# Optimization experiments

Hardware: AMD Instinct MI355X
Metric: run time of the kernel (lower is better)

The kernel has to match this reference:

```python
import jax, jax.numpy as jnp
import numpy as np
import math

B, S, DM, H = 4, 2048, 1024, 16
HD = DM // H

def setup_inputs() -> dict:
    key = jax.random.key(0)
    ks = jax.random.split(key, 12)
    def lin(k, din, dout):
        bound = 1.0 / math.sqrt(din)
        kw, kb = jax.random.split(k)
        W = jax.random.uniform(kw, (din, dout), jnp.float32, -bound, bound)
        b = jax.random.uniform(kb, (dout,), jnp.float32, -bound, bound)
        return W, b
    Wq, bq = lin(ks[0], DM, DM)
    Wk, bk = lin(ks[1], DM, DM)
    Wv, bv = lin(ks[2], DM, DM)
    Wo, bo = lin(ks[3], DM, DM)
    return {
        "Q": jax.random.normal(ks[4], (B, S, DM), jnp.float32),
        "K": jax.random.normal(ks[5], (B, S, DM), jnp.float32),
        "V": jax.random.normal(ks[6], (B, S, DM), jnp.float32),
        "mask": jnp.ones((B, S), jnp.int32),
        "Wq": Wq, "bq": bq, "Wk": Wk, "bk": bk,
        "Wv": Wv, "bv": bv, "Wo": Wo, "bo": bo,
    }

def reference(Q, K, V, mask, Wq, bq, Wk, bk, Wv, bv, Wo, bo):
    N, qlen, dm = Q.shape
    klen = K.shape[1]
    q = (Q @ Wq + bq).reshape(N, qlen, H, HD)
    k = (K @ Wk + bk).reshape(N, klen, H, HD)
    v = (V @ Wv + bv).reshape(N, klen, H, HD)
    # scores: [B, q, H, k]
    dot = jnp.einsum('bqhd,bkhd->bqhk', q, k) / math.sqrt(HD)
    # mask is 2-D (N, klen): broadcast as (N, 1, 1, klen); positions where mask==0 are masked
    m = (mask == 0)[:, None, None, :]
    dot = jnp.where(m, -jnp.inf, dot)
    weights = jax.nn.softmax(dot.astype(jnp.float32), axis=-1).astype(dot.dtype)
    out = jnp.einsum('bqhk,bkhd->bqhd', weights, v).reshape(N, qlen, dm)
    return out @ Wo + bo
```

## Files before the change

kernel.cpp:

```cpp
#include <hip/hip_runtime.h>
#include <math.h>

#define B_  4
#define S_  2048
#define DM_ 1024
#define H_  16
#define HD_ 64

typedef float f32x4 __attribute__((ext_vector_type(4)));
typedef short bf16x8 __attribute__((ext_vector_type(8)));

#define MFMA16(a, b, c) __builtin_amdgcn_mfma_f32_16x16x32_bf16((a), (b), (c), 0, 0, 0)

static __device__ __forceinline__ unsigned short f2bf(float f) {
    union { float f; unsigned int i; } c; c.f = f;
    unsigned int u = c.i;
    return (unsigned short)((u + 0x7fffu + ((u >> 16) & 1u)) >> 16);
}
static __device__ __forceinline__ unsigned int f2u(float f) {
    union { float f; unsigned int u; } c; c.f = f; return c.u;
}
static __device__ __forceinline__ float u2f(unsigned int u) {
    union { unsigned int u; float f; } c; c.u = u; return c.f;
}

static __device__ __forceinline__ void async16(const void* g, void* l) {
    __builtin_amdgcn_global_load_lds(
        (__attribute__((address_space(1))) void*)(void*)g,
        (__attribute__((address_space(3))) void*)l, 16, 0, 0);
}

__global__ __launch_bounds__(256) void cast3_bf16(
    const float* __restrict__ q, const float* __restrict__ k,
    const float* __restrict__ v,
    unsigned short* __restrict__ qo, unsigned short* __restrict__ ko,
    unsigned short* __restrict__ vo) {
    const int z = blockIdx.z;
    const float* in = z == 0 ? q : (z == 1 ? k : v);
    unsigned short* out = z == 0 ? qo : (z == 1 ? ko : vo);
    int idx = (blockIdx.x * 256 + threadIdx.x) * 8;
    float4 a = *(const float4*)(in + idx);
    float4 b = *(const float4*)(in + idx + 4);
    *(ushort4*)(out + idx)     = make_ushort4(f2bf(a.x), f2bf(a.y), f2bf(a.z), f2bf(a.w));
    *(ushort4*)(out + idx + 4) = make_ushort4(f2bf(b.x), f2bf(b.y), f2bf(b.z), f2bf(b.w));
}

__global__ __launch_bounds__(256) void wcast4_t(
    const float* __restrict__ w0, const float* __restrict__ w1,
    const float* __restrict__ w2, const float* __restrict__ w3,
    unsigned short* __restrict__ o0, unsigned short* __restrict__ o1,
    unsigned short* __restrict__ o2, unsigned short* __restrict__ o3) {
    __shared__ float tile[64][65];
    const int z = blockIdx.z;
    const float* W = z == 0 ? w0 : (z == 1 ? w1 : (z == 2 ? w2 : w3));
    unsigned short* Wt = z == 0 ? o0 : (z == 1 ? o1 : (z == 2 ? o2 : o3));
    const int t = threadIdx.x;
    const int k0 = blockIdx.y * 64, n0 = blockIdx.x * 64;
    const int r = t >> 4, c4 = (t & 15) * 4;
    #pragma unroll
    for (int s = 0; s < 4; ++s) {
        float4 f = *(const float4*)(W + (size_t)(k0 + s * 16 + r) * DM_ + n0 + c4);
        tile[s * 16 + r][c4 + 0] = f.x; tile[s * 16 + r][c4 + 1] = f.y;
        tile[s * 16 + r][c4 + 2] = f.z; tile[s * 16 + r][c4 + 3] = f.w;
    }
    __syncthreads();
    #pragma unroll
    for (int s = 0; s < 4; ++s) {
        int n = s * 16 + r;
        ushort4 o = make_ushort4(f2bf(tile[c4 + 0][n]), f2bf(tile[c4 + 1][n]),
                                 f2bf(tile[c4 + 2][n]), f2bf(tile[c4 + 3][n]));
        *(ushort4*)(Wt + (size_t)(n0 + n) * DM_ + k0 + c4) = o;
    }
}

static __device__ __forceinline__ void gemm_body(
    const unsigned short* __restrict__ A,
    const unsigned short* __restrict__ Wt,
    const float* __restrict__ bias,
    void* __restrict__ outp, int mode,
    unsigned short* As, unsigned short* Bs)
{
    const int t = threadIdx.x;
    const int w = t >> 6, l = t & 63;
    const int quad = l >> 4, l16 = l & 15;
    const int wr = w >> 1, wc = w & 1;
    const int m0 = blockIdx.y * 128, n0 = blockIdx.x * 128;

    const int srow = w * 32 + (l >> 2);
    const int scol = (l & 3) * 8;
    const unsigned short* ag = A  + (size_t)(m0 + srow) * DM_ + scol;
    const unsigned short* bg = Wt + (size_t)(n0 + srow) * DM_ + scol;
    unsigned short* al = &As[(w * 32) * 32];
    unsigned short* bl = &Bs[(w * 32) * 32];

    const f32x4 fz = {0.f, 0.f, 0.f, 0.f};
    f32x4 acc[4][4];
    #pragma unroll
    for (int i = 0; i < 4; ++i)
        #pragma unroll
        for (int j = 0; j < 4; ++j) acc[i][j] = fz;

    for (int k0 = 0; k0 < DM_; k0 += 32) {
        __syncthreads();
        async16(ag + k0, al);
        async16(ag + k0 + 16 * DM_, al + 16 * 32);
        async16(bg + k0, bl);
        async16(bg + k0 + 16 * DM_, bl + 16 * 32);
        __syncthreads();
        bf16x8 af[4], bfr[4];
        #pragma unroll
        for (int i = 0; i < 4; ++i)
            af[i] = *(const bf16x8*)&As[(wr * 64 + i * 16 + l16) * 32 + quad * 8];
        #pragma unroll
        for (int j = 0; j < 4; ++j)
            bfr[j] = *(const bf16x8*)&Bs[(wc * 64 + j * 16 + l16) * 32 + quad * 8];
        #pragma unroll
        for (int i = 0; i < 4; ++i)
            #pragma unroll
            for (int j = 0; j < 4; ++j)
                acc[i][j] = MFMA16(af[i], bfr[j], acc[i][j]);
    }

    float bv[4];
    #pragma unroll
    for (int j = 0; j < 4; ++j) bv[j] = bias[n0 + wc * 64 + j * 16 + l16];

    if (mode == 2) {
        float* out = (float*)outp;
        #pragma unroll
        for (int i = 0; i < 4; ++i)
            #pragma unroll
            for (int j = 0; j < 4; ++j) {
                int col = n0 + wc * 64 + j * 16 + l16;
                #pragma unroll
                for (int r = 0; r < 4; ++r) {
                    int row = m0 + wr * 64 + i * 16 + quad * 4 + r;
                    out[(size_t)row * DM_ + col] = acc[i][j][r] + bv[j];
                }
            }
    } else if (mode == 0) {
        unsigned short* out = (unsigned short*)outp;
        #pragma unroll
        for (int i = 0; i < 4; ++i)
            #pragma unroll
            for (int j = 0; j < 4; ++j) {
                int col = n0 + wc * 64 + j * 16 + l16;
                int h = col >> 6, d = col & 63;
                #pragma unroll
                for (int r = 0; r < 4; ++r) {
                    int row = m0 + wr * 64 + i * 16 + quad * 4 + r;
                    int bb = row >> 11, ss = row & (S_ - 1);
                    out[(((size_t)bb * H_ + h) * S_ + ss) * HD_ + d] =
                        f2bf(acc[i][j][r] + bv[j]);
                }
            }
    } else {
        unsigned short* out = (unsigned short*)outp;
        #pragma unroll
        for (int i = 0; i < 4; ++i)
            #pragma unroll
            for (int j = 0; j < 4; ++j) {
                int col = n0 + wc * 64 + j * 16 + l16;
                int h = col >> 6, d = col & 63;
                int row0 = m0 + wr * 64 + i * 16 + quad * 4;
                int bb = row0 >> 11, ss = row0 & (S_ - 1);
                ushort4 o = make_ushort4(f2bf(acc[i][j][0] + bv[j]),
                                         f2bf(acc[i][j][1] + bv[j]),
                                         f2bf(acc[i][j][2] + bv[j]),
                                         f2bf(acc[i][j][3] + bv[j]));
                *(ushort4*)(out + (((size_t)bb * H_ + h) * HD_ + d) * S_ + ss) = o;
            }
    }
}

__global__ __launch_bounds__(256) void gemm_qkv3(
    const unsigned short* __restrict__ Qc, const unsigned short* __restrict__ Kc,
    const unsigned short* __restrict__ Vc,
    const unsigned short* __restrict__ Wqt, const unsigned short* __restrict__ Wkt,
    const unsigned short* __restrict__ Wvt,
    const float* __restrict__ bq, const float* __restrict__ bk,
    const float* __restrict__ bvp,
    unsigned short* __restrict__ qh, unsigned short* __restrict__ kh,
    unsigned short* __restrict__ vth)
{
    __shared__ unsigned short As[128 * 32];
    __shared__ unsigned short Bs[128 * 32];
    const int z = blockIdx.z;
    const unsigned short* A  = z == 0 ? Qc  : (z == 1 ? Kc  : Vc);
    const unsigned short* Wt = z == 0 ? Wqt : (z == 1 ? Wkt : Wvt);
    const float* bias        = z == 0 ? bq  : (z == 1 ? bk  : bvp);
    void* out                = z == 0 ? (void*)qh : (z == 1 ? (void*)kh : (void*)vth);
    gemm_body(A, Wt, bias, out, z == 2 ? 1 : 0, As, Bs);
}

__global__ __launch_bounds__(256) void gemm_omfma(
    const unsigned short* __restrict__ A, const unsigned short* __restrict__ Wt,
    const float* __restrict__ bias, float* __restrict__ out)
{
    __shared__ unsigned short As[128 * 32];
    __shared__ unsigned short Bs[128 * 32];
    gemm_body(A, Wt, bias, out, 2, As, Bs);
}

__global__ __launch_bounds__(256) void attn_mfma(
    const unsigned short* __restrict__ q,
    const unsigned short* __restrict__ k,
    const unsigned short* __restrict__ vt,
    const int* __restrict__ mask,
    unsigned short* __restrict__ out)
{
    __shared__ unsigned short Qs[128 * 64];
    __shared__ unsigned short Ks[64 * 64];
    __shared__ unsigned short Vs[64 * 64];
    __shared__ unsigned short Ps[4][2][16 * 64];
    __shared__ int ms[64];
    const int t = threadIdx.x;
    const int w = t >> 6, l = t & 63;
    const int quad = l >> 4, l16 = l & 15;
    const int b = blockIdx.z, h = blockIdx.y;
    const int q0 = blockIdx.x * 128;
    const size_t hb = ((size_t)b * H_ + h) * S_;
    const float C_ = 0.18033688011112042f;
    const float NINF = -__builtin_inff();

    const unsigned short* qg = q + (hb + q0) * HD_;
    #pragma unroll
    for (int s = 0; s < 4; ++s) {
        int r0 = w * 32 + s * 8;
        int row = r0 + (l >> 3);
        int g = (l & 7) ^ (row & 7);
        async16(qg + (size_t)row * HD_ + g * 8, &Qs[r0 * 64]);
    }
    __syncthreads();
    bf16x8 qf[2][2];
    #pragma unroll
    for (int g = 0; g < 2; ++g)
        #pragma unroll
        for (int c = 0; c < 2; ++c) {
            int row = w * 32 + g * 16 + l16;
            qf[g][c] = *(const bf16x8*)&Qs[row * 64 + (((c * 4 + quad) ^ (row & 7)) * 8)];
        }

    const f32x4 fz = {0.f, 0.f, 0.f, 0.f};
    f32x4 o[2][4];
    float lr[2] = {0.f, 0.f};
    #pragma unroll
    for (int g = 0; g < 2; ++g)
        #pragma unroll
        for (int jv = 0; jv < 4; ++jv) o[g][jv] = fz;

    const unsigned short* kg0 = k + hb * HD_;
    const unsigned short* vg0 = vt + ((size_t)b * H_ + h) * HD_ * S_;

    for (int kt = 0; kt < S_ / 64; ++kt) {
        __syncthreads();
        #pragma unroll
        for (int s = 0; s < 2; ++s) {
            int r0 = w * 16 + s * 8;
            int rr = r0 + (l >> 3);
            int gg = (l & 7) ^ (rr & 7);
            async16(kg0 + (size_t)(kt * 64 + rr) * HD_ + gg * 8, &Ks[r0 * 64]);
            async16(vg0 + (size_t)rr * S_ + kt * 64 + gg * 8, &Vs[r0 * 64]);
        }
        if (t < 64) ms[t] = mask[(size_t)b * S_ + kt * 64 + t];
        __syncthreads();

        float madd[4][4];
        #pragma unroll
        for (int kk = 0; kk < 4; ++kk) {
            int4 mv = *(const int4*)&ms[kk * 16 + quad * 4];
            madd[kk][0] = mv.x ? 0.f : NINF;
            madd[kk][1] = mv.y ? 0.f : NINF;
            madd[kk][2] = mv.z ? 0.f : NINF;
            madd[kk][3] = mv.w ? 0.f : NINF;
        }

        bf16x8 kf[4][2], vfr[4][2];
        #pragma unroll
        for (int kk = 0; kk < 4; ++kk) {
            int row = kk * 16 + l16;
            #pragma unroll
            for (int c = 0; c < 2; ++c)
                kf[kk][c] = *(const bf16x8*)&Ks[row * 64 + (((c * 4 + quad) ^ (row & 7)) * 8)];
        }
        #pragma unroll
        for (int jv = 0; jv < 4; ++jv) {
            int row = jv * 16 + l16;
            #pragma unroll
            for (int c = 0; c < 2; ++c)
                vfr[jv][c] = *(const bf16x8*)&Vs[row * 64 + (((c * 4 + quad) ^ (row & 7)) * 8)];
        }

        #pragma unroll
        for (int g = 0; g < 2; ++g) {
            f32x4 sc[4];
            #pragma unroll
            for (int kk = 0; kk < 4; ++kk) sc[kk] = fz;
            #pragma unroll
            for (int kk = 0; kk < 4; ++kk) {
                sc[kk] = MFMA16(kf[kk][0], qf[g][0], sc[kk]);
                sc[kk] = MFMA16(kf[kk][1], qf[g][1], sc[kk]);
            }
            unsigned short* Pg = &Ps[w][g][0];
            float lacc = 0.f;
            #pragma unroll
            for (int kk = 0; kk < 4; ++kk) {
                #pragma unroll
                for (int rp = 0; rp < 2; ++rp) {
                    float p0 = exp2f(fmaf(sc[kk][rp * 2 + 0], C_, madd[kk][rp * 2 + 0]));
                    float p1 = exp2f(fmaf(sc[kk][rp * 2 + 1], C_, madd[kk][rp * 2 + 1]));
                    unsigned int pk = __builtin_amdgcn_perm(f2u(p1), f2u(p0), 0x07060302u);
                    lacc += u2f(pk << 16);
                    lacc += u2f(pk & 0xffff0000u);
                    int kb = (kk * 2 + (quad >> 1)) ^ (l16 & 7);
                    *(unsigned int*)&Pg[l16 * 64 + kb * 8 + (quad & 1) * 4 + rp * 2] = pk;
                }
            }
            lr[g] += lacc;
            bf16x8 pa0 = *(const bf16x8*)&Pg[l16 * 64 + ((quad ^ (l16 & 7)) * 8)];
            bf16x8 pa1 = *(const bf16x8*)&Pg[l16 * 64 + (((4 + quad) ^ (l16 & 7)) * 8)];
            #pragma unroll
            for (int jv = 0; jv < 4; ++jv) {
                o[g][jv] = MFMA16(pa0, vfr[jv][0], o[g][jv]);
                o[g][jv] = MFMA16(pa1, vfr[jv][1], o[g][jv]);
            }
        }
    }
    #pragma unroll
    for (int g = 0; g < 2; ++g) {
        float ls = lr[g];
        ls += __shfl_xor(ls, 16);
        ls += __shfl_xor(ls, 32);
        float inv = 1.0f / ls;
        float invr[4];
        #pragma unroll
        for (int r = 0; r < 4; ++r)
            invr[r] = __shfl(inv, (l & 48) | (quad * 4 + r));
        #pragma unroll
        for (int jv = 0; jv < 4; ++jv) {
            int col = h * HD_ + jv * 16 + l16;
            #pragma unroll
            for (int r = 0; r < 4; ++r) {
                int row = q0 + w * 32 + g * 16 + quad * 4 + r;
                out[((size_t)b * S_ + row) * DM_ + col] = f2bf(o[g][jv][r] * invr[r]);
            }
        }
    }
}

extern "C" void kernel_launch(void* const* d_in, const int* in_sizes, int n_in,
                              void* d_out, int out_size, void* d_ws, size_t ws_size,
                              hipStream_t stream) {
    const float* Q    = (const float*)d_in[0];
    const float* K    = (const float*)d_in[1];
    const float* V    = (const float*)d_in[2];
    const int*   mask = (const int*)d_in[3];
    const float* Wq   = (const float*)d_in[4];
    const float* bq   = (const float*)d_in[5];
    const float* Wk   = (const float*)d_in[6];
    const float* bk   = (const float*)d_in[7];
    const float* Wv   = (const float*)d_in[8];
    const float* bv   = (const float*)d_in[9];
    const float* Wo   = (const float*)d_in[10];
    const float* bo   = (const float*)d_in[11];

    char* ws = (char*)d_ws;
    const size_t MB = 1024 * 1024;
    unsigned short* Qc  = (unsigned short*)(ws);
    unsigned short* Kc  = (unsigned short*)(ws + 16 * MB);
    unsigned short* Vc  = (unsigned short*)(ws + 32 * MB);
    unsigned short* Wqt = (unsigned short*)(ws + 48 * MB);
    unsigned short* Wkt = (unsigned short*)(ws + 50 * MB);
    unsigned short* Wvt = (unsigned short*)(ws + 52 * MB);
    unsigned short* Wot = (unsigned short*)(ws + 54 * MB);
    unsigned short* qh  = (unsigned short*)(ws + 56 * MB);
    unsigned short* kh  = (unsigned short*)(ws + 72 * MB);
    unsigned short* vth = (unsigned short*)(ws + 88 * MB);
    unsigned short* ao  = (unsigned short*)(ws + 104 * MB);

    cast3_bf16<<<dim3(4096, 1, 3), 256, 0, stream>>>(Q, K, V, Qc, Kc, Vc);
    wcast4_t<<<dim3(16, 16, 4), 256, 0, stream>>>(Wq, Wk, Wv, Wo, Wqt, Wkt, Wvt, Wot);
    gemm_qkv3<<<dim3(DM_ / 128, (B_ * S_) / 128, 3), 256, 0, stream>>>(
        Qc, Kc, Vc, Wqt, Wkt, Wvt, bq, bk, bv, qh, kh, vth);
    attn_mfma<<<dim3(S_ / 128, H_, B_), 256, 0, stream>>>(qh, kh, vth, mask, ao);
    gemm_omfma<<<dim3(DM_ / 128, (B_ * S_) / 128), 256, 0, stream>>>(ao, Wot, bo, (float*)d_out);
}
```

Baseline: 411.6 us.

## Widen GEMM K-tile to 64 with XOR-swizzled LDS and trim attention softmax ops

```diff
diff --git a/kernel.cpp b/kernel.cpp
--- a/kernel.cpp
+++ b/kernel.cpp
@@ -19,9 +19,6 @@
 }
 static __device__ __forceinline__ unsigned int f2u(float f) {
     union { float f; unsigned int u; } c; c.f = f; return c.u;
-}
-static __device__ __forceinline__ float u2f(unsigned int u) {
-    union { unsigned int u; float f; } c; c.u = u; return c.f;
 }
 
 static __device__ __forceinline__ void async16(const void* g, void* l) {
@@ -86,12 +83,10 @@
     const int wr = w >> 1, wc = w & 1;
     const int m0 = blockIdx.y * 128, n0 = blockIdx.x * 128;
 
-    const int srow = w * 32 + (l >> 2);
-    const int scol = (l & 3) * 8;
-    const unsigned short* ag = A  + (size_t)(m0 + srow) * DM_ + scol;
-    const unsigned short* bg = Wt + (size_t)(n0 + srow) * DM_ + scol;
-    unsigned short* al = &As[(w * 32) * 32];
-    unsigned short* bl = &Bs[(w * 32) * 32];
+    const int srow8 = l >> 3;
+    const int sch   = (l & 7) ^ srow8;
+    const unsigned short* ag = A  + (size_t)(m0 + w * 32 + srow8) * DM_ + sch * 8;
+    const unsigned short* bg = Wt + (size_t)(n0 + w * 32 + srow8) * DM_ + sch * 8;
 
     const f32x4 fz = {0.f, 0.f, 0.f, 0.f};
     f32x4 acc[4][4];
@@ -100,25 +95,31 @@
         #pragma unroll
         for (int j = 0; j < 4; ++j) acc[i][j] = fz;
 
-    for (int k0 = 0; k0 < DM_; k0 += 32) {
+    const int rsw = l16 & 7;
+    for (int k0 = 0; k0 < DM_; k0 += 64) {
         __syncthreads();
-        async16(ag + k0, al);
-        async16(ag + k0 + 16 * DM_, al + 16 * 32);
-        async16(bg + k0, bl);
-        async16(bg + k0 + 16 * DM_, bl + 16 * 32);
+        #pragma unroll
+        for (int s = 0; s < 4; ++s) {
+            async16(ag + k0 + (size_t)(s * 8) * DM_, &As[(w * 32 + s * 8) * 64]);
+            async16(bg + k0 + (size_t)(s * 8) * DM_, &Bs[(w * 32 + s * 8) * 64]);
+        }
         __syncthreads();
-        bf16x8 af[4], bfr[4];
-        #pragma unroll
-        for (int i = 0; i < 4; ++i)
-            af[i] = *(const bf16x8*)&As[(wr * 64 + i * 16 + l16) * 32 + quad * 8];
-        #pragma unroll
-        for (int j = 0; j < 4; ++j)
-            bfr[j] = *(const bf16x8*)&Bs[(wc * 64 + j * 16 + l16) * 32 + quad * 8];
-        #pragma unroll
-        for (int i = 0; i < 4; ++i)
+        #pragma unroll
+        for (int c = 0; c < 2; ++c) {
+            const int csw = ((c * 4 + quad) ^ rsw) * 8;
+            bf16x8 af[4], bfr[4];
+            #pragma unroll
+            for (int i = 0; i < 4; ++i)
+                af[i] = *(const bf16x8*)&As[(wr * 64 + i * 16 + l16) * 64 + csw];
             #pragma unroll
             for (int j = 0; j < 4; ++j)
-                acc[i][j] = MFMA16(af[i], bfr[j], acc[i][j]);
+                bfr[j] = *(const bf16x8*)&Bs[(wc * 64 + j * 16 + l16) * 64 + csw];
+            #pragma unroll
+            for (int i = 0; i < 4; ++i)
+                #pragma unroll
+                for (int j = 0; j < 4; ++j)
+                    acc[i][j] = MFMA16(af[i], bfr[j], acc[i][j]);
+        }
     }
 
     float bv[4];
@@ -183,8 +184,8 @@
     unsigned short* __restrict__ qh, unsigned short* __restrict__ kh,
     unsigned short* __restrict__ vth)
 {
-    __shared__ unsigned short As[128 * 32];
-    __shared__ unsigned short Bs[128 * 32];
+    __shared__ unsigned short As[128 * 64];
+    __shared__ unsigned short Bs[128 * 64];
     const int z = blockIdx.z;
     const unsigned short* A  = z == 0 ? Qc  : (z == 1 ? Kc  : Vc);
     const unsigned short* Wt = z == 0 ? Wqt : (z == 1 ? Wkt : Wvt);
@@ -197,8 +198,8 @@
     const unsigned short* __restrict__ A, const unsigned short* __restrict__ Wt,
     const float* __restrict__ bias, float* __restrict__ out)
 {
-    __shared__ unsigned short As[128 * 32];
-    __shared__ unsigned short Bs[128 * 32];
+    __shared__ unsigned short As[128 * 64];
+    __shared__ unsigned short Bs[128 * 64];
     gemm_body(A, Wt, bias, out, 2, As, Bs);
 }
 
@@ -213,7 +214,7 @@
     __shared__ unsigned short Ks[64 * 64];
     __shared__ unsigned short Vs[64 * 64];
     __shared__ unsigned short Ps[4][2][16 * 64];
-    __shared__ int ms[64];
+    __shared__ float msf[64];
     const int t = threadIdx.x;
     const int w = t >> 6, l = t & 63;
     const int quad = l >> 4, l16 = l & 15;
@@ -223,13 +224,14 @@
     const float C_ = 0.18033688011112042f;
     const float NINF = -__builtin_inff();
 
+    const int srow8 = l >> 3;
+    const int sch   = (l & 7) ^ srow8;
+
     const unsigned short* qg = q + (hb + q0) * HD_;
     #pragma unroll
     for (int s = 0; s < 4; ++s) {
         int r0 = w * 32 + s * 8;
-        int row = r0 + (l >> 3);
-        int g = (l & 7) ^ (row & 7);
-        async16(qg + (size_t)row * HD_ + g * 8, &Qs[r0 * 64]);
+        async16(qg + (size_t)(r0 + srow8) * HD_ + sch * 8, &Qs[r0 * 64]);
     }
     __syncthreads();
     bf16x8 qf[2][2];
@@ -251,28 +253,26 @@
 
     const unsigned short* kg0 = k + hb * HD_;
     const unsigned short* vg0 = vt + ((size_t)b * H_ + h) * HD_ * S_;
+    const int rsw = l16 & 7;
 
     for (int kt = 0; kt < S_ / 64; ++kt) {
         __syncthreads();
         #pragma unroll
         for (int s = 0; s < 2; ++s) {
             int r0 = w * 16 + s * 8;
-            int rr = r0 + (l >> 3);
-            int gg = (l & 7) ^ (rr & 7);
-            async16(kg0 + (size_t)(kt * 64 + rr) * HD_ + gg * 8, &Ks[r0 * 64]);
-            async16(vg0 + (size_t)rr * S_ + kt * 64 + gg * 8, &Vs[r0 * 64]);
-        }
-        if (t < 64) ms[t] = mask[(size_t)b * S_ + kt * 64 + t];
+            int rr = r0 + srow8;
+            async16(kg0 + (size_t)(kt * 64 + rr) * HD_ + sch * 8, &Ks[r0 * 64]);
+            async16(vg0 + (size_t)rr * S_ + kt * 64 + sch * 8, &Vs[r0 * 64]);
+        }
+        if (t < 64) msf[t] = mask[(size_t)b * S_ + kt * 64 + t] ? 0.f : NINF;
         __syncthreads();
 
         float madd[4][4];
         #pragma unroll
         for (int kk = 0; kk < 4; ++kk) {
-            int4 mv = *(const int4*)&ms[kk * 16 + quad * 4];
-            madd[kk][0] = mv.x ? 0.f : NINF;
-            madd[kk][1] = mv.y ? 0.f : NINF;
-            madd[kk][2] = mv.z ? 0.f : NINF;
-            madd[kk][3] = mv.w ? 0.f : NINF;
+            float4 mv = *(const float4*)&msf[kk * 16 + quad * 4];
+            madd[kk][0] = mv.x; madd[kk][1] = mv.y;
+            madd[kk][2] = mv.z; madd[kk][3] = mv.w;
         }
 
         bf16x8 kf[4][2], vfr[4][2];
@@ -281,14 +281,14 @@
             int row = kk * 16 + l16;
             #pragma unroll
             for (int c = 0; c < 2; ++c)
-                kf[kk][c] = *(const bf16x8*)&Ks[row * 64 + (((c * 4 + quad) ^ (row & 7)) * 8)];
+                kf[kk][c] = *(const bf16x8*)&Ks[row * 64 + (((c * 4 + quad) ^ rsw) * 8)];
         }
         #pragma unroll
         for (int jv = 0; jv < 4; ++jv) {
             int row = jv * 16 + l16;
             #pragma unroll
             for (int c = 0; c < 2; ++c)
-                vfr[jv][c] = *(const bf16x8*)&Vs[row * 64 + (((c * 4 + quad) ^ (row & 7)) * 8)];
+                vfr[jv][c] = *(const bf16x8*)&Vs[row * 64 + (((c * 4 + quad) ^ rsw) * 8)];
         }
 
         #pragma unroll
@@ -305,20 +305,21 @@
             float lacc = 0.f;
             #pragma unroll
             for (int kk = 0; kk < 4; ++kk) {
+                int kb = (kk * 2 + (quad >> 1)) ^ rsw;
                 #pragma unroll
                 for (int rp = 0; rp < 2; ++rp) {
-                    float p0 = exp2f(fmaf(sc[kk][rp * 2 + 0], C_, madd[kk][rp * 2 + 0]));
-                    float p1 = exp2f(fmaf(sc[kk][rp * 2 + 1], C_, madd[kk][rp * 2 + 1]));
+                    float p0 = __builtin_amdgcn_exp2f(
+                        fmaf(sc[kk][rp * 2 + 0], C_, madd[kk][rp * 2 + 0]));
+                    float p1 = __builtin_amdgcn_exp2f(
+                        fmaf(sc[kk][rp * 2 + 1], C_, madd[kk][rp * 2 + 1]));
                     unsigned int pk = __builtin_amdgcn_perm(f2u(p1), f2u(p0), 0x07060302u);
-                    lacc += u2f(pk << 16);
-                    lacc += u2f(pk & 0xffff0000u);
-                    int kb = (kk * 2 + (quad >> 1)) ^ (l16 & 7);
+                    lacc += p0 + p1;
                     *(unsigned int*)&Pg[l16 * 64 + kb * 8 + (quad & 1) * 4 + rp * 2] = pk;
                 }
             }
             lr[g] += lacc;
-            bf16x8 pa0 = *(const bf16x8*)&Pg[l16 * 64 + ((quad ^ (l16 & 7)) * 8)];
-            bf16x8 pa1 = *(const bf16x8*)&Pg[l16 * 64 + (((4 + quad) ^ (l16 & 7)) * 8)];
+            bf16x8 pa0 = *(const bf16x8*)&Pg[l16 * 64 + ((quad ^ rsw) * 8)];
+            bf16x8 pa1 = *(const bf16x8*)&Pg[l16 * 64 + (((4 + quad) ^ rsw) * 8)];
             #pragma unroll
             for (int jv = 0; jv < 4; ++jv) {
                 o[g][jv] = MFMA16(pa0, vfr[jv][0], o[g][jv]);
```

After: 358.7 us. -12.8%, faster.
